# Kernel tuning notes

Measured on AMD Instinct MI355X. Metric: run time of the kernel, lower is better.

## Reference

```python
import jax, jax.numpy as jnp
import numpy as np

# Mamba block dims (config: d_model=1024, expand=2, d_state=16, d_conv=4, dt_rank=auto)
D_MODEL = 1024
D_INNER = 2048
D_STATE = 16
D_CONV = 4
DT_RANK = 64
B_SZ = 2
SEQ = 2048
EPS = 1e-5
DT_MIN, DT_MAX, DT_FLOOR = 0.001, 0.1, 1e-4


def setup_inputs() -> dict:
    key = jax.random.key(0)
    ks = jax.random.split(key, 8)
    s = 0.02  # initializer_range
    # dt_proj bias init: inverse-softplus of dt sampled log-uniform in [dt_min, dt_max]
    dt = jnp.exp(jax.random.uniform(ks[6], (D_INNER,)) * (np.log(DT_MAX) - np.log(DT_MIN)) + np.log(DT_MIN))
    dt = jnp.clip(dt, DT_FLOOR, None)
    inv_dt = dt + jnp.log(-jnp.expm1(-dt))
    A_init = jnp.broadcast_to(jnp.arange(1, D_STATE + 1, dtype=jnp.float32), (D_INNER, D_STATE))
    return {
        "hidden_states": jax.random.normal(ks[0], (B_SZ, SEQ, D_MODEL), jnp.float32),
        "norm_weight": jnp.ones((D_MODEL,), jnp.float32),
        "in_proj_w": jax.random.normal(ks[1], (2 * D_INNER, D_MODEL), jnp.float32) * s,
        "conv_w": jax.random.normal(ks[2], (D_INNER, 1, D_CONV), jnp.float32) * s,
        "conv_b": jnp.zeros((D_INNER,), jnp.float32),
        "x_proj_w": jax.random.normal(ks[3], (DT_RANK + 2 * D_STATE, D_INNER), jnp.float32) * s,
        "dt_proj_w": jax.random.normal(ks[4], (D_INNER, DT_RANK), jnp.float32) * s,
        "dt_proj_b": inv_dt,
        "A_log": jnp.log(A_init),
        "D": jnp.ones((D_INNER,), jnp.float32),
        "out_proj_w": jax.random.normal(ks[5], (D_MODEL, D_INNER), jnp.float32) * s,
    }


def reference(hidden_states, norm_weight, in_proj_w, conv_w, conv_b, x_proj_w,
              dt_proj_w, dt_proj_b, A_log, D, out_proj_w):
    residual = hidden_states
    # RMSNorm
    h = hidden_states * jax.lax.rsqrt(jnp.mean(hidden_states * hidden_states, -1, keepdims=True) + EPS)
    h = h * norm_weight
    # input projection -> x (ssm branch) and z (gate)
    xz = h @ in_proj_w.T                      # [B, L, 2*d_inner]
    x, z = jnp.split(xz, 2, axis=-1)
    # causal depthwise conv over time
    xc = x.transpose(0, 2, 1)                 # [B, d_inner, L]
    xc = jax.lax.conv_general_dilated(
        xc, conv_w, window_strides=(1,), padding=[(D_CONV - 1, 0)],
        feature_group_count=D_INNER, dimension_numbers=("NCH", "OIH", "NCH"))
    xc = xc + conv_b[None, :, None]
    x = jax.nn.silu(xc.transpose(0, 2, 1))    # [B, L, d_inner]
    # data-dependent SSM params
    dbl = x @ x_proj_w.T                      # [B, L, dt_rank + 2*d_state]
    dt_r = dbl[..., :DT_RANK]
    Bm = dbl[..., DT_RANK:DT_RANK + D_STATE]  # [B, L, N]
    Cm = dbl[..., DT_RANK + D_STATE:]         # [B, L, N]
    dt = jax.nn.softplus(dt_r @ dt_proj_w.T + dt_proj_b)  # [B, L, d_inner]
    A = -jnp.exp(A_log)                       # [d_inner, N], negative

    def step(hstate, inputs):
        x_t, dt_t, B_t, C_t = inputs          # [B,d],[B,d],[B,N],[B,N]
        dA = jnp.exp(dt_t[..., None] * A)     # [B, d, N]
        hstate = hstate * dA + (dt_t * x_t)[..., None] * B_t[:, None, :]
        y_t = jnp.einsum("bdn,bn->bd", hstate, C_t)
        return hstate, y_t

    xs = (x.transpose(1, 0, 2), dt.transpose(1, 0, 2),
          Bm.transpose(1, 0, 2), Cm.transpose(1, 0, 2))
    h0 = jnp.zeros((hidden_states.shape[0], D_INNER, D_STATE), x.dtype)
    _, ys = jax.lax.scan(step, h0, xs)        # ys: [L, B, d_inner]
    y = ys.transpose(1, 0, 2) + x * D
    y = y * jax.nn.silu(z)                    # gated output
    return y @ out_proj_w.T + residual
```

## Files before the change

kernel.cpp:

```cpp
#include <hip/hip_runtime.h>
#include <math.h>

#define D_MODEL 1024
#define D_INNER 2048
#define D_STATE 16
#define D_CONV  4
#define DT_RANK 64
#define B_SZ    2
#define SEQ     2048
#define NTOK    (B_SZ*SEQ)
#define DBL_N   (DT_RANK + 2*D_STATE)
#define CHUNK   64
#define NCHUNK  (SEQ/CHUNK)

typedef __attribute__((ext_vector_type(8))) short short8;
typedef __attribute__((ext_vector_type(4))) float f32x4;

__device__ __forceinline__ unsigned short f2bf(float f) {
    union { float f; unsigned int u; } v; v.f = f;
    unsigned int r = v.u + 0x7fff + ((v.u >> 16) & 1);
    return (unsigned short)(r >> 16);
}
__device__ __forceinline__ float bf2f(unsigned short u) {
    union { unsigned int u; float f; } v; v.u = ((unsigned int)u) << 16;
    return v.f;
}

__global__ __launch_bounds__(256) void rmsnorm_kernel(
    const float* __restrict__ h, const float* __restrict__ w, unsigned short* __restrict__ out)
{
    int tok = blockIdx.x;
    const float4* row = (const float4*)(h + (size_t)tok * D_MODEL);
    float4 v = row[threadIdx.x];
    float ss = v.x*v.x + v.y*v.y + v.z*v.z + v.w*v.w;
    #pragma unroll
    for (int off = 32; off >= 1; off >>= 1) ss += __shfl_down(ss, off, 64);
    __shared__ float red[4];
    int wave = threadIdx.x >> 6, lane = threadIdx.x & 63;
    if (lane == 0) red[wave] = ss;
    __syncthreads();
    float tot = red[0] + red[1] + red[2] + red[3];
    float scale = rsqrtf(tot * (1.0f / D_MODEL) + 1e-5f);
    float4 wv = ((const float4*)w)[threadIdx.x];
    ushort4 o;
    o.x = f2bf(v.x * scale * wv.x);
    o.y = f2bf(v.y * scale * wv.y);
    o.z = f2bf(v.z * scale * wv.z);
    o.w = f2bf(v.w * scale * wv.w);
    ((ushort4*)(out + (size_t)tok * D_MODEL))[threadIdx.x] = o;
}

__global__ __launch_bounds__(256) void cast_bf16_kernel(
    const float4* __restrict__ in, ushort4* __restrict__ out, int n4)
{
    int i = blockIdx.x * 256 + threadIdx.x;
    if (i < n4) {
        float4 v = in[i];
        ushort4 o; o.x = f2bf(v.x); o.y = f2bf(v.y); o.z = f2bf(v.z); o.w = f2bf(v.w);
        out[i] = o;
    }
}

__global__ __launch_bounds__(256) void mfma_gemm_kernel(
    const unsigned short* __restrict__ A, int lda,
    const unsigned short* __restrict__ W, int ldw,
    float* __restrict__ C, int ldc,
    unsigned short* __restrict__ Cbf, int ldcbf,
    int kLen, int Nmax,
    const float* __restrict__ bias,
    const float* __restrict__ add, int ldadd,
    int act, size_t segStride)
{
    __shared__ __align__(16) unsigned short As[128 * 32];
    __shared__ __align__(16) unsigned short Bs[128 * 32];
    const int bm = blockIdx.y * 128;
    const int bn = blockIdx.x * 128;
    const int kBeg = blockIdx.z * kLen;
    const int tid = threadIdx.x;
    const int lane = tid & 63;
    const int wave = tid >> 6;
    const int wm = (wave >> 1) * 64;
    const int wn = (wave & 1) * 64;
    const int frow = lane & 15;
    const int quad = lane >> 4;
    const int sw = (frow >> 1) & 3;

    if (C) C += blockIdx.z * segStride;

    f32x4 acc[4][4];
    #pragma unroll
    for (int i = 0; i < 4; ++i)
        #pragma unroll
        for (int j = 0; j < 4; ++j)
            acc[i][j] = (f32x4){0.f, 0.f, 0.f, 0.f};

    for (int k0 = kBeg; k0 < kBeg + kLen; k0 += 32) {
        __syncthreads();
        #pragma unroll
        for (int i = 0; i < 2; ++i) {
            int q = (wave * 2 + i) * 64 + lane;
            int r = q >> 2, cl = q & 3;
            int cg = cl ^ ((r >> 1) & 3);
            const unsigned short* ga = A + (size_t)(bm + r) * lda + k0 + cg * 8;
            const unsigned short* gb = W + (size_t)(bn + r) * ldw + k0 + cg * 8;
            __builtin_amdgcn_global_load_lds(
                (const __attribute__((address_space(1))) void*)ga,
                (__attribute__((address_space(3))) void*)(As + (wave * 2 + i) * 512),
                16, 0, 0);
            __builtin_amdgcn_global_load_lds(
                (const __attribute__((address_space(1))) void*)gb,
                (__attribute__((address_space(3))) void*)(Bs + (wave * 2 + i) * 512),
                16, 0, 0);
        }
        __syncthreads();
        short8 af[4], bf[4];
        #pragma unroll
        for (int i = 0; i < 4; ++i)
            af[i] = *(const short8*)&As[(wm + i * 16 + frow) * 32 + (quad ^ sw) * 8];
        #pragma unroll
        for (int j = 0; j < 4; ++j)
            bf[j] = *(const short8*)&Bs[(wn + j * 16 + frow) * 32 + (quad ^ sw) * 8];
        #pragma unroll
        for (int i = 0; i < 4; ++i)
            #pragma unroll
            for (int j = 0; j < 4; ++j)
                acc[i][j] = __builtin_amdgcn_mfma_f32_16x16x32_bf16(
                    af[i], bf[j], acc[i][j], 0, 0, 0);
    }

    #pragma unroll
    for (int i = 0; i < 4; ++i) {
        #pragma unroll
        for (int r = 0; r < 4; ++r) {
            int row = bm + wm + i * 16 + quad * 4 + r;
            #pragma unroll
            for (int j = 0; j < 4; ++j) {
                int col = bn + wn + j * 16 + frow;
                if (col < Nmax) {
                    float v = acc[i][j][r];
                    if (bias) v += bias[col];
                    if (act == 1) v = (v > 20.0f) ? v : log1pf(__expf(v));
                    if (add) v += add[(size_t)row * ldadd + col];
                    if (C)   C[(size_t)row * ldc + col] = v;
                    if (Cbf) Cbf[(size_t)row * ldcbf + col] = f2bf(v);
                }
            }
        }
    }
}

__global__ __launch_bounds__(256) void reduce_xproj_kernel(
    const float* __restrict__ part, float* __restrict__ dbl,
    unsigned short* __restrict__ dtr)
{
    const int N = NTOK * DBL_N;
    int idx = blockIdx.x * 256 + threadIdx.x;
    if (idx >= N) return;
    float s = part[idx] + part[idx + N] + part[idx + 2 * N] + part[idx + 3 * N];
    dbl[idx] = s;
    unsigned int col = (unsigned int)idx % DBL_N;
    if (col < DT_RANK) {
        unsigned int tok = (unsigned int)idx / DBL_N;
        dtr[(size_t)tok * DT_RANK + col] = f2bf(s);
    }
}

__global__ __launch_bounds__(256) void conv_silu_kernel(
    const unsigned short* __restrict__ xz, const float* __restrict__ cw,
    const float* __restrict__ cb, unsigned short* __restrict__ out_bf)
{
    int idx = blockIdx.x * 256 + threadIdx.x;
    int d = idx & (D_INNER - 1);
    int t = (idx >> 11) & (SEQ - 1);
    int b = idx >> 22;
    const unsigned short* xcol = xz + (size_t)b * SEQ * (2 * D_INNER) + d;
    float w0 = cw[d * 4 + 0], w1 = cw[d * 4 + 1], w2 = cw[d * 4 + 2], w3 = cw[d * 4 + 3];
    float acc = cb[d];
    if (t >= 3) acc = fmaf(bf2f(xcol[(size_t)(t - 3) * (2 * D_INNER)]), w0, acc);
    if (t >= 2) acc = fmaf(bf2f(xcol[(size_t)(t - 2) * (2 * D_INNER)]), w1, acc);
    if (t >= 1) acc = fmaf(bf2f(xcol[(size_t)(t - 1) * (2 * D_INNER)]), w2, acc);
    acc = fmaf(bf2f(xcol[(size_t)t * (2 * D_INNER)]), w3, acc);
    float sig = 1.0f / (1.0f + __expf(-acc));
    out_bf[(size_t)(b * SEQ + t) * D_INNER + d] = f2bf(acc * sig);
}

__global__ __launch_bounds__(256) void scan_phase1_kernel(
    const float* __restrict__ dtb, const unsigned short* __restrict__ xconv,
    const float* __restrict__ dbl, const float* __restrict__ A_log,
    float* __restrict__ sum_a, float* __restrict__ sum_h)
{
    const int d = blockIdx.y * 256 + threadIdx.x;
    const int c = blockIdx.x;
    const int b = blockIdx.z;
    const int t0 = c * CHUNK;

    float An[D_STATE];
    bool fast = true;
    #pragma unroll
    for (int n = 0; n < D_STATE; ++n) {
        An[n] = -__expf(A_log[d * D_STATE + n]);
        fast = fast && (fabsf(An[n] + (float)(n + 1)) < 2e-3f);
    }
    const float* dt_p = dtb + ((size_t)b * SEQ + t0) * D_INNER + d;
    const unsigned short* x_p = xconv + ((size_t)b * SEQ + t0) * D_INNER + d;
    const float* Brow = dbl + ((size_t)b * SEQ + t0) * DBL_N + DT_RANK;

    float h[D_STATE];
    #pragma unroll
    for (int n = 0; n < D_STATE; ++n) h[n] = 0.f;
    float sumdt = 0.f;

    if (fast) {
        for (int t = 0; t < CHUNK; ++t) {
            float dt = dt_p[(size_t)t * D_INNER];
            float xv = bf2f(x_p[(size_t)t * D_INNER]);
            const float4* B4 = (const float4*)(Brow + (size_t)t * DBL_N);
            float4 b0 = B4[0], b1 = B4[1], b2 = B4[2], b3 = B4[3];
            float Bv[16] = {b0.x,b0.y,b0.z,b0.w, b1.x,b1.y,b1.z,b1.w,
                            b2.x,b2.y,b2.z,b2.w, b3.x,b3.y,b3.z,b3.w};
            sumdt += dt;
            float e1 = __expf(-dt);
            float dtx = dt * xv;
            float ea = 1.f;
            #pragma unroll
            for (int n = 0; n < D_STATE; ++n) {
                ea *= e1;
                h[n] = fmaf(h[n], ea, dtx * Bv[n]);
            }
        }
    } else {
        for (int t = 0; t < CHUNK; ++t) {
            float dt = dt_p[(size_t)t * D_INNER];
            float xv = bf2f(x_p[(size_t)t * D_INNER]);
            const float4* B4 = (const float4*)(Brow + (size_t)t * DBL_N);
            float4 b0 = B4[0], b1 = B4[1], b2 = B4[2], b3 = B4[3];
            float Bv[16] = {b0.x,b0.y,b0.z,b0.w, b1.x,b1.y,b1.z,b1.w,
                            b2.x,b2.y,b2.z,b2.w, b3.x,b3.y,b3.z,b3.w};
            sumdt += dt;
            float dtx = dt * xv;
            #pragma unroll
            for (int n = 0; n < D_STATE; ++n) {
                float ea = __expf(dt * An[n]);
                h[n] = fmaf(h[n], ea, dtx * Bv[n]);
            }
        }
    }

    float a[D_STATE];
    if (fast) {
        float E = __expf(-sumdt);
        float ea = 1.f;
        #pragma unroll
        for (int n = 0; n < D_STATE; ++n) { ea *= E; a[n] = ea; }
    } else {
        #pragma unroll
        for (int n = 0; n < D_STATE; ++n) a[n] = __expf(An[n] * sumdt);
    }
    size_t base = (((size_t)b * D_INNER + d) * NCHUNK + c) * D_STATE;
    #pragma unroll
    for (int i = 0; i < 4; ++i) {
        ((float4*)(sum_a + base))[i] = (float4){a[4*i], a[4*i+1], a[4*i+2], a[4*i+3]};
        ((float4*)(sum_h + base))[i] = (float4){h[4*i], h[4*i+1], h[4*i+2], h[4*i+3]};
    }
}

__global__ __launch_bounds__(256) void scan_carry_kernel(
    const float* __restrict__ sum_a, float* __restrict__ sum_h)
{
    size_t g = (size_t)blockIdx.x * 256 + threadIdx.x;
    size_t bd = g >> 4;
    int n = (int)(g & 15);
    size_t base = bd * NCHUNK * D_STATE + n;
    float hh = 0.f;
    for (int c = 0; c < NCHUNK; ++c) {
        size_t idx = base + (size_t)c * D_STATE;
        float a = sum_a[idx];
        float hp = sum_h[idx];
        sum_h[idx] = hh;
        hh = fmaf(hh, a, hp);
    }
}

__global__ __launch_bounds__(256) void scan_phase3_kernel(
    const float* __restrict__ dtb, const unsigned short* __restrict__ xconv,
    const unsigned short* __restrict__ xz, const float* __restrict__ dbl,
    const float* __restrict__ A_log, const float* __restrict__ Dvec,
    const float* __restrict__ hinit, unsigned short* __restrict__ y)
{
    const int d = blockIdx.y * 256 + threadIdx.x;
    const int c = blockIdx.x;
    const int b = blockIdx.z;
    const int t0 = c * CHUNK;

    float An[D_STATE];
    bool fast = true;
    #pragma unroll
    for (int n = 0; n < D_STATE; ++n) {
        An[n] = -__expf(A_log[d * D_STATE + n]);
        fast = fast && (fabsf(An[n] + (float)(n + 1)) < 2e-3f);
    }
    const float Dd = Dvec[d];
    const float* dt_p = dtb + ((size_t)b * SEQ + t0) * D_INNER + d;
    const unsigned short* x_p = xconv + ((size_t)b * SEQ + t0) * D_INNER + d;
    const unsigned short* z_p = xz + ((size_t)b * SEQ + t0) * (2 * D_INNER) + D_INNER + d;
    const float* Brow = dbl + ((size_t)b * SEQ + t0) * DBL_N + DT_RANK;
    unsigned short* y_p = y + ((size_t)b * SEQ + t0) * D_INNER + d;

    size_t base = (((size_t)b * D_INNER + d) * NCHUNK + c) * D_STATE;
    float h[D_STATE];
    #pragma unroll
    for (int i = 0; i < 4; ++i) {
        float4 hv = ((const float4*)(hinit + base))[i];
        h[4*i] = hv.x; h[4*i+1] = hv.y; h[4*i+2] = hv.z; h[4*i+3] = hv.w;
    }

    if (fast) {
        for (int t = 0; t < CHUNK; ++t) {
            float dt = dt_p[(size_t)t * D_INNER];
            float xv = bf2f(x_p[(size_t)t * D_INNER]);
            const float4* B4 = (const float4*)(Brow + (size_t)t * DBL_N);
            float4 b0 = B4[0], b1 = B4[1], b2 = B4[2], b3 = B4[3];
            float4 c0 = B4[4], c1 = B4[5], c2 = B4[6], c3 = B4[7];
            float Bv[16] = {b0.x,b0.y,b0.z,b0.w, b1.x,b1.y,b1.z,b1.w,
                            b2.x,b2.y,b2.z,b2.w, b3.x,b3.y,b3.z,b3.w};
            float Cv[16] = {c0.x,c0.y,c0.z,c0.w, c1.x,c1.y,c1.z,c1.w,
                            c2.x,c2.y,c2.z,c2.w, c3.x,c3.y,c3.z,c3.w};
            float e1 = __expf(-dt);
            float dtx = dt * xv;
            float ea = 1.f, yy = 0.f;
            #pragma unroll
            for (int n = 0; n < D_STATE; ++n) {
                ea *= e1;
                h[n] = fmaf(h[n], ea, dtx * Bv[n]);
                yy = fmaf(h[n], Cv[n], yy);
            }
            float zv = bf2f(z_p[(size_t)t * (2 * D_INNER)]);
            float sig = 1.0f / (1.0f + __expf(-zv));
            y_p[(size_t)t * D_INNER] = f2bf((yy + xv * Dd) * (zv * sig));
        }
    } else {
        for (int t = 0; t < CHUNK; ++t) {
            float dt = dt_p[(size_t)t * D_INNER];
            float xv = bf2f(x_p[(size_t)t * D_INNER]);
            const float4* B4 = (const float4*)(Brow + (size_t)t * DBL_N);
            float4 b0 = B4[0], b1 = B4[1], b2 = B4[2], b3 = B4[3];
            float4 c0 = B4[4], c1 = B4[5], c2 = B4[6], c3 = B4[7];
            float Bv[16] = {b0.x,b0.y,b0.z,b0.w, b1.x,b1.y,b1.z,b1.w,
                            b2.x,b2.y,b2.z,b2.w, b3.x,b3.y,b3.z,b3.w};
            float Cv[16] = {c0.x,c0.y,c0.z,c0.w, c1.x,c1.y,c1.z,c1.w,
                            c2.x,c2.y,c2.z,c2.w, c3.x,c3.y,c3.z,c3.w};
            float dtx = dt * xv;
            float yy = 0.f;
            #pragma unroll
            for (int n = 0; n < D_STATE; ++n) {
                float ea = __expf(dt * An[n]);
                h[n] = fmaf(h[n], ea, dtx * Bv[n]);
                yy = fmaf(h[n], Cv[n], yy);
            }
            float zv = bf2f(z_p[(size_t)t * (2 * D_INNER)]);
            float sig = 1.0f / (1.0f + __expf(-zv));
            y_p[(size_t)t * D_INNER] = f2bf((yy + xv * Dd) * (zv * sig));
        }
    }
}

extern "C" void kernel_launch(void* const* d_in, const int* in_sizes, int n_in,
                              void* d_out, int out_size, void* d_ws, size_t ws_size,
                              hipStream_t stream) {
    const float* hs        = (const float*)d_in[0];
    const float* norm_w    = (const float*)d_in[1];
    const float* in_proj_w = (const float*)d_in[2];
    const float* conv_w    = (const float*)d_in[3];
    const float* conv_b    = (const float*)d_in[4];
    const float* x_proj_w  = (const float*)d_in[5];
    const float* dt_proj_w = (const float*)d_in[6];
    const float* dt_proj_b = (const float*)d_in[7];
    const float* A_log     = (const float*)d_in[8];
    const float* Dvec      = (const float*)d_in[9];
    const float* out_proj_w= (const float*)d_in[10];
    float* out = (float*)d_out;

    float* wsf      = (float*)d_ws;
    float* dbl      = wsf;
    float* dbl_part = dbl      + (size_t)393216;
    float* dtb      = dbl_part + (size_t)1572864;
    float* sum_a    = dtb      + (size_t)8388608;
    float* sum_h    = sum_a    + (size_t)2097152;
    unsigned short* xz_bf    = (unsigned short*)(sum_h + 2097152);
    unsigned short* xconv_bf = xz_bf    + (size_t)16777216;
    unsigned short* hnorm_bf = xconv_bf + (size_t)8388608;
    unsigned short* ybuf_bf  = hnorm_bf + (size_t)4194304;
    unsigned short* wi_bf    = ybuf_bf  + (size_t)8388608;
    unsigned short* wo_bf    = wi_bf    + (size_t)4194304;
    unsigned short* wx_bf    = wo_bf    + (size_t)2097152;
    unsigned short* wdt_bf   = wx_bf    + (size_t)262144;
    unsigned short* dtr_bf   = wdt_bf   + (size_t)131072;

    cast_bf16_kernel<<<(2 * D_INNER * D_MODEL / 4 + 255) / 256, 256, 0, stream>>>(
        (const float4*)in_proj_w, (ushort4*)wi_bf, 2 * D_INNER * D_MODEL / 4);
    cast_bf16_kernel<<<(D_MODEL * D_INNER / 4 + 255) / 256, 256, 0, stream>>>(
        (const float4*)out_proj_w, (ushort4*)wo_bf, D_MODEL * D_INNER / 4);
    cast_bf16_kernel<<<(DBL_N * D_INNER / 4 + 255) / 256, 256, 0, stream>>>(
        (const float4*)x_proj_w, (ushort4*)wx_bf, DBL_N * D_INNER / 4);
    cast_bf16_kernel<<<(D_INNER * DT_RANK / 4 + 255) / 256, 256, 0, stream>>>(
        (const float4*)dt_proj_w, (ushort4*)wdt_bf, D_INNER * DT_RANK / 4);

    rmsnorm_kernel<<<NTOK, 256, 0, stream>>>(hs, norm_w, hnorm_bf);
    mfma_gemm_kernel<<<dim3((2 * D_INNER) / 128, NTOK / 128), 256, 0, stream>>>(
        hnorm_bf, D_MODEL, wi_bf, D_MODEL, nullptr, 0, xz_bf, 2 * D_INNER,
        D_MODEL, 2 * D_INNER, nullptr, nullptr, 0, 0, 0);
    conv_silu_kernel<<<(NTOK * D_INNER) / 256, 256, 0, stream>>>(
        xz_bf, conv_w, conv_b, xconv_bf);
    mfma_gemm_kernel<<<dim3(1, NTOK / 128, 4), 256, 0, stream>>>(
        xconv_bf, D_INNER, wx_bf, D_INNER, dbl_part, DBL_N, nullptr, 0,
        D_INNER / 4, DBL_N, nullptr, nullptr, 0, 0, (size_t)NTOK * DBL_N);
    reduce_xproj_kernel<<<(NTOK * DBL_N + 255) / 256, 256, 0, stream>>>(
        dbl_part, dbl, dtr_bf);
    mfma_gemm_kernel<<<dim3(D_INNER / 128, NTOK / 128), 256, 0, stream>>>(
        dtr_bf, DT_RANK, wdt_bf, DT_RANK, dtb, D_INNER, nullptr, 0,
        DT_RANK, D_INNER, dt_proj_b, nullptr, 0, 1, 0);
    scan_phase1_kernel<<<dim3(NCHUNK, D_INNER / 256, B_SZ), 256, 0, stream>>>(
        dtb, xconv_bf, dbl, A_log, sum_a, sum_h);
    scan_carry_kernel<<<(B_SZ * D_INNER * D_STATE) / 256, 256, 0, stream>>>(sum_a, sum_h);
    scan_phase3_kernel<<<dim3(NCHUNK, D_INNER / 256, B_SZ), 256, 0, stream>>>(
        dtb, xconv_bf, xz_bf, dbl, A_log, Dvec, sum_h, ybuf_bf);
    mfma_gemm_kernel<<<dim3(D_MODEL / 128, NTOK / 128), 256, 0, stream>>>(
        ybuf_bf, D_INNER, wo_bf, D_INNER, out, D_MODEL, nullptr, 0,
        D_INNER, D_MODEL, nullptr, hs, D_MODEL, 0, 0);
}
```

Baseline: 403.2 us.

## Pre-swizzle GEMM operands in global memory and merge weight casts into one launch

Each producer kernel (rmsnorm, weight cast, conv, x_proj reduce, scan output) now writes its bf16 output with the XOR chunk swizzle baked into the column address. The GEMM can then load contiguous 16-byte chunks without computing the swizzle. The four weight-cast launches are merged into one kernel. The scan kernels read x and write y through the swizzled indices, which adds index arithmetic in the inner loop and must stay consistent across every producer and consumer.

```diff
diff --git a/kernel.cpp b/kernel.cpp
--- a/kernel.cpp
+++ b/kernel.cpp
@@ -24,6 +24,10 @@
 __device__ __forceinline__ float bf2f(unsigned short u) {
     union { unsigned int u; float f; } v; v.u = ((unsigned int)u) << 16;
     return v.f;
+}
+__device__ __forceinline__ int swz_col(int r, int k) {
+    int p = (((k >> 3) ^ (r >> 1)) & 3) << 3;
+    return (k & ~0x18) | p;
 }
 
 __global__ __launch_bounds__(256) void rmsnorm_kernel(
@@ -47,18 +51,29 @@
     o.y = f2bf(v.y * scale * wv.y);
     o.z = f2bf(v.z * scale * wv.z);
     o.w = f2bf(v.w * scale * wv.w);
-    ((ushort4*)(out + (size_t)tok * D_MODEL))[threadIdx.x] = o;
-}
-
-__global__ __launch_bounds__(256) void cast_bf16_kernel(
-    const float4* __restrict__ in, ushort4* __restrict__ out, int n4)
+    int col = swz_col(tok, threadIdx.x * 4);
+    *(ushort4*)(out + (size_t)tok * D_MODEL + col) = o;
+}
+
+__global__ __launch_bounds__(256) void cast4_swz_kernel(
+    const float4* __restrict__ s0, unsigned short* __restrict__ d0, int n0, int l0,
+    const float4* __restrict__ s1, unsigned short* __restrict__ d1, int n1, int l1,
+    const float4* __restrict__ s2, unsigned short* __restrict__ d2, int n2, int l2,
+    const float4* __restrict__ s3, unsigned short* __restrict__ d3, int n3, int l3)
 {
     int i = blockIdx.x * 256 + threadIdx.x;
-    if (i < n4) {
-        float4 v = in[i];
-        ushort4 o; o.x = f2bf(v.x); o.y = f2bf(v.y); o.z = f2bf(v.z); o.w = f2bf(v.w);
-        out[i] = o;
-    }
+    const float4* s; unsigned short* d; int ll;
+    if (i < n0) { s = s0; d = d0; ll = l0; }
+    else if ((i -= n0) < n1) { s = s1; d = d1; ll = l1; }
+    else if ((i -= n1) < n2) { s = s2; d = d2; ll = l2; }
+    else if ((i -= n2) < n3) { s = s3; d = d3; ll = l3; }
+    else return;
+    int e = i * 4;
+    int r = e >> ll;
+    int k = e & ((1 << ll) - 1);
+    float4 v = s[i];
+    ushort4 o; o.x = f2bf(v.x); o.y = f2bf(v.y); o.z = f2bf(v.z); o.w = f2bf(v.w);
+    *(ushort4*)(d + ((size_t)r << ll) + swz_col(r, k)) = o;
 }
 
 __global__ __launch_bounds__(256) void mfma_gemm_kernel(
@@ -100,9 +115,8 @@
         for (int i = 0; i < 2; ++i) {
             int q = (wave * 2 + i) * 64 + lane;
             int r = q >> 2, cl = q & 3;
-            int cg = cl ^ ((r >> 1) & 3);
-            const unsigned short* ga = A + (size_t)(bm + r) * lda + k0 + cg * 8;
-            const unsigned short* gb = W + (size_t)(bn + r) * ldw + k0 + cg * 8;
+            const unsigned short* ga = A + (size_t)(bm + r) * lda + k0 + cl * 8;
+            const unsigned short* gb = W + (size_t)(bn + r) * ldw + k0 + cl * 8;
             __builtin_amdgcn_global_load_lds(
                 (const __attribute__((address_space(1))) void*)ga,
                 (__attribute__((address_space(3))) void*)(As + (wave * 2 + i) * 512),
@@ -161,7 +175,7 @@
     unsigned int col = (unsigned int)idx % DBL_N;
     if (col < DT_RANK) {
         unsigned int tok = (unsigned int)idx / DBL_N;
-        dtr[(size_t)tok * DT_RANK + col] = f2bf(s);
+        dtr[(size_t)tok * DT_RANK + swz_col((int)tok, (int)col)] = f2bf(s);
     }
 }
 
@@ -181,7 +195,7 @@
     if (t >= 1) acc = fmaf(bf2f(xcol[(size_t)(t - 1) * (2 * D_INNER)]), w2, acc);
     acc = fmaf(bf2f(xcol[(size_t)t * (2 * D_INNER)]), w3, acc);
     float sig = 1.0f / (1.0f + __expf(-acc));
-    out_bf[(size_t)(b * SEQ + t) * D_INNER + d] = f2bf(acc * sig);
+    out_bf[(size_t)(b * SEQ + t) * D_INNER + swz_col(t, d)] = f2bf(acc * sig);
 }
 
 __global__ __launch_bounds__(256) void scan_phase1_kernel(
@@ -193,6 +207,8 @@
     const int c = blockIdx.x;
     const int b = blockIdx.z;
     const int t0 = c * CHUNK;
+    const int dbase = d & ~0x18;
+    const int dch = (d >> 3) & 3;
 
     float An[D_STATE];
     bool fast = true;
@@ -202,7 +218,7 @@
         fast = fast && (fabsf(An[n] + (float)(n + 1)) < 2e-3f);
     }
     const float* dt_p = dtb + ((size_t)b * SEQ + t0) * D_INNER + d;
-    const unsigned short* x_p = xconv + ((size_t)b * SEQ + t0) * D_INNER + d;
+    const unsigned short* xrow = xconv + ((size_t)b * SEQ + t0) * D_INNER;
     const float* Brow = dbl + ((size_t)b * SEQ + t0) * DBL_N + DT_RANK;
 
     float h[D_STATE];
@@ -213,7 +229,8 @@
     if (fast) {
         for (int t = 0; t < CHUNK; ++t) {
             float dt = dt_p[(size_t)t * D_INNER];
-            float xv = bf2f(x_p[(size_t)t * D_INNER]);
+            int xcol = dbase | (((dch ^ (t >> 1)) & 3) << 3);
+            float xv = bf2f(xrow[(size_t)t * D_INNER + xcol]);
             const float4* B4 = (const float4*)(Brow + (size_t)t * DBL_N);
             float4 b0 = B4[0], b1 = B4[1], b2 = B4[2], b3 = B4[3];
             float Bv[16] = {b0.x,b0.y,b0.z,b0.w, b1.x,b1.y,b1.z,b1.w,
@@ -231,7 +248,8 @@
     } else {
         for (int t = 0; t < CHUNK; ++t) {
             float dt = dt_p[(size_t)t * D_INNER];
-            float xv = bf2f(x_p[(size_t)t * D_INNER]);
+            int xcol = dbase | (((dch ^ (t >> 1)) & 3) << 3);
+            float xv = bf2f(xrow[(size_t)t * D_INNER + xcol]);
             const float4* B4 = (const float4*)(Brow + (size_t)t * DBL_N);
             float4 b0 = B4[0], b1 = B4[1], b2 = B4[2], b3 = B4[3];
             float Bv[16] = {b0.x,b0.y,b0.z,b0.w, b1.x,b1.y,b1.z,b1.w,
@@ -291,6 +309,8 @@
     const int c = blockIdx.x;
     const int b = blockIdx.z;
     const int t0 = c * CHUNK;
+    const int dbase = d & ~0x18;
+    const int dch = (d >> 3) & 3;
 
     float An[D_STATE];
     bool fast = true;
@@ -301,10 +321,10 @@
     }
     const float Dd = Dvec[d];
     const float* dt_p = dtb + ((size_t)b * SEQ + t0) * D_INNER + d;
-    const unsigned short* x_p = xconv + ((size_t)b * SEQ + t0) * D_INNER + d;
+    const unsigned short* xrow = xconv + ((size_t)b * SEQ + t0) * D_INNER;
     const unsigned short* z_p = xz + ((size_t)b * SEQ + t0) * (2 * D_INNER) + D_INNER + d;
     const float* Brow = dbl + ((size_t)b * SEQ + t0) * DBL_N + DT_RANK;
-    unsigned short* y_p = y + ((size_t)b * SEQ + t0) * D_INNER + d;
+    unsigned short* yrow = y + ((size_t)b * SEQ + t0) * D_INNER;
 
     size_t base = (((size_t)b * D_INNER + d) * NCHUNK + c) * D_STATE;
     float h[D_STATE];
@@ -317,7 +337,8 @@
     if (fast) {
         for (int t = 0; t < CHUNK; ++t) {
             float dt = dt_p[(size_t)t * D_INNER];
-            float xv = bf2f(x_p[(size_t)t * D_INNER]);
+            int xcol = dbase | (((dch ^ (t >> 1)) & 3) << 3);
+            float xv = bf2f(xrow[(size_t)t * D_INNER + xcol]);
             const float4* B4 = (const float4*)(Brow + (size_t)t * DBL_N);
             float4 b0 = B4[0], b1 = B4[1], b2 = B4[2], b3 = B4[3];
             float4 c0 = B4[4], c1 = B4[5], c2 = B4[6], c3 = B4[7];
@@ -336,12 +357,13 @@
             }
             float zv = bf2f(z_p[(size_t)t * (2 * D_INNER)]);
             float sig = 1.0f / (1.0f + __expf(-zv));
-            y_p[(size_t)t * D_INNER] = f2bf((yy + xv * Dd) * (zv * sig));
+            yrow[(size_t)t * D_INNER + xcol] = f2bf((yy + xv * Dd) * (zv * sig));
         }
     } else {
         for (int t = 0; t < CHUNK; ++t) {
             float dt = dt_p[(size_t)t * D_INNER];
-            float xv = bf2f(x_p[(size_t)t * D_INNER]);
+            int xcol = dbase | (((dch ^ (t >> 1)) & 3) << 3);
+            float xv = bf2f(xrow[(size_t)t * D_INNER + xcol]);
             const float4* B4 = (const float4*)(Brow + (size_t)t * DBL_N);
             float4 b0 = B4[0], b1 = B4[1], b2 = B4[2], b3 = B4[3];
             float4 c0 = B4[4], c1 = B4[5], c2 = B4[6], c3 = B4[7];
@@ -359,7 +381,7 @@
             }
             float zv = bf2f(z_p[(size_t)t * (2 * D_INNER)]);
             float sig = 1.0f / (1.0f + __expf(-zv));
-            y_p[(size_t)t * D_INNER] = f2bf((yy + xv * Dd) * (zv * sig));
+            yrow[(size_t)t * D_INNER + xcol] = f2bf((yy + xv * Dd) * (zv * sig));
         }
     }
 }
@@ -396,14 +418,18 @@
     unsigned short* wdt_bf   = wx_bf    + (size_t)262144;
     unsigned short* dtr_bf   = wdt_bf   + (size_t)131072;
 
-    cast_bf16_kernel<<<(2 * D_INNER * D_MODEL / 4 + 255) / 256, 256, 0, stream>>>(
-        (const float4*)in_proj_w, (ushort4*)wi_bf, 2 * D_INNER * D_MODEL / 4);
-    cast_bf16_kernel<<<(D_MODEL * D_INNER / 4 + 255) / 256, 256, 0, stream>>>(
-        (const float4*)out_proj_w, (ushort4*)wo_bf, D_MODEL * D_INNER / 4);
-    cast_bf16_kernel<<<(DBL_N * D_INNER / 4 + 255) / 256, 256, 0, stream>>>(
-        (const float4*)x_proj_w, (ushort4*)wx_bf, DBL_N * D_INNER / 4);
-    cast_bf16_kernel<<<(D_INNER * DT_RANK / 4 + 255) / 256, 256, 0, stream>>>(
-        (const float4*)dt_proj_w, (ushort4*)wdt_bf, D_INNER * DT_RANK / 4);
+    {
+        int n0 = 2 * D_INNER * D_MODEL / 4;
+        int n1 = D_MODEL * D_INNER / 4;
+        int n2 = DBL_N * D_INNER / 4;
+        int n3 = D_INNER * DT_RANK / 4;
+        int tot = n0 + n1 + n2 + n3;
+        cast4_swz_kernel<<<(tot + 255) / 256, 256, 0, stream>>>(
+            (const float4*)in_proj_w,  wi_bf,  n0, 10,
+            (const float4*)out_proj_w, wo_bf,  n1, 11,
+            (const float4*)x_proj_w,   wx_bf,  n2, 11,
+            (const float4*)dt_proj_w,  wdt_bf, n3, 6);
+    }
 
     rmsnorm_kernel<<<NTOK, 256, 0, stream>>>(hs, norm_w, hnorm_bf);
     mfma_gemm_kernel<<<dim3((2 * D_INNER) / 128, NTOK / 128), 256, 0, stream>>>(
```

After: 400.7 us. No clear change (-0.6%).
